# Optimization experiments

Hardware: AMD Instinct MI355X
Metric: run time of the kernel (lower is better)

The kernel has to match this reference:

```python
import jax, jax.numpy as jnp
import numpy as np

N = 50000        # nodes
E = 800000       # edges (before self-loops)
IN = 128         # in_channels
HID = 32         # hidden_channels
HEADS = 8        # num_heads
G = 64           # num graphs in batch
NEG_SLOPE = 0.2  # PyG GATConv default


def setup_inputs() -> dict:
    key = jax.random.key(0)
    ks = jax.random.split(key, 12)
    x = jax.random.normal(ks[0], (N, IN), jnp.float32)
    edge_index = jax.random.randint(ks[1], (2, E), 0, N, jnp.int32)
    edge_attr = jax.random.normal(ks[2], (E, 4), jnp.float32)
    batch = jnp.sort(jax.random.randint(ks[3], (N,), 0, G, jnp.int32))
    s = 0.05
    # GATConv 1: in -> HEADS*HID
    W1 = jax.random.normal(ks[4], (IN, HEADS * HID), jnp.float32) * s
    a_src1 = jax.random.normal(ks[5], (HEADS, HID), jnp.float32) * s
    a_dst1 = jax.random.normal(ks[6], (HEADS, HID), jnp.float32) * s
    b1 = jnp.zeros((HEADS * HID,), jnp.float32)
    # GATConv 2: HEADS*HID -> HID (heads=1)
    W2 = jax.random.normal(ks[7], (HEADS * HID, HID), jnp.float32) * s
    a_src2 = jax.random.normal(ks[8], (1, HID), jnp.float32) * s
    a_dst2 = jax.random.normal(ks[9], (1, HID), jnp.float32) * s
    b2 = jnp.zeros((HID,), jnp.float32)
    return {"x": x, "edge_index": edge_index, "edge_attr": edge_attr, "batch": batch,
            "W1": W1, "a_src1": a_src1, "a_dst1": a_dst1, "b1": b1,
            "W2": W2, "a_src2": a_src2, "a_dst2": a_dst2, "b2": b2}


def gat_conv(x, src, dst, W, a_src, a_dst, b):
    # x: [N, F_in]; W: [F_in, H*C]; a_src/a_dst: [H, C]
    H, C = a_src.shape
    h = (x @ W).reshape(N, H, C)                      # [N, H, C]
    al_s = jnp.einsum('nhc,hc->nh', h, a_src)         # [N, H]
    al_d = jnp.einsum('nhc,hc->nh', h, a_dst)
    e = jax.nn.leaky_relu(al_s[src] + al_d[dst], NEG_SLOPE)  # [Etot, H]
    # segment softmax over incoming edges of each dst node
    m = jax.ops.segment_max(e, dst, num_segments=N)
    p = jnp.exp(e - m[dst])
    z = jax.ops.segment_sum(p, dst, num_segments=N)
    alpha = p / z[dst]                                # [Etot, H]
    out = jax.ops.segment_sum(alpha[:, :, None] * h[src], dst, num_segments=N)
    return out.reshape(N, H * C) + b


def reference(x, edge_index, edge_attr, batch, W1, a_src1, a_dst1, b1, W2, a_src2, a_dst2, b2):
    # edge_attr is ignored: GATConv was built without edge_dim (PyG lin_edge=None).
    loops = jnp.arange(N, dtype=edge_index.dtype)     # PyG add_self_loops=True
    src = jnp.concatenate([edge_index[0], loops])
    dst = jnp.concatenate([edge_index[1], loops])
    h = jax.nn.relu(gat_conv(x, src, dst, W1, a_src1, a_dst1, b1))
    # dropout p=0.2 is identity in eval mode
    h = gat_conv(h, src, dst, W2, a_src2, a_dst2, b2)  # [N, HID]
    # global_mean_pool over graph ids
    sums = jax.ops.segment_sum(h, batch, num_segments=G)
    cnts = jax.ops.segment_sum(jnp.ones((N, 1), h.dtype), batch, num_segments=G)
    return sums / jnp.maximum(cnts, 1.0)              # [G, HID]
```

## Files before the change

### kernel.cpp

```cpp
#include <hip/hip_runtime.h>
#include <hip/hip_bf16.h>

#define NNODES 50000
#define NEDGES 800000
#define FIN 128
#define HID 32
#define HEADS 8
#define NG 64
#define NEG_SLOPE 0.2f
#define MAXDEG 64
#define NPX 6250

using bf16x8 = __attribute__((ext_vector_type(8))) short;
using f32x4  = __attribute__((ext_vector_type(4))) float;
using f32x2  = __attribute__((ext_vector_type(2))) float;

static __device__ __forceinline__ float leaky(float x) {
    return x > 0.f ? x : NEG_SLOPE * x;
}
static __device__ __forceinline__ unsigned short f2bf(float f) {
    unsigned int x = __float_as_uint(f);
    return (unsigned short)((x + 0x7FFFu + ((x >> 16) & 1u)) >> 16);
}
static __device__ __forceinline__ unsigned int pack2bf(float lo, float hi) {
    return (unsigned int)f2bf(lo) | ((unsigned int)f2bf(hi) << 16);
}
static __device__ __forceinline__ float bfl(unsigned int u) {
    return __uint_as_float(u << 16);
}
static __device__ __forceinline__ float bfh(unsigned int u) {
    return __uint_as_float(u & 0xFFFF0000u);
}
static __device__ __forceinline__ unsigned char f2fp8(float f) {
    return (unsigned char)(__builtin_amdgcn_cvt_pk_fp8_f32(f, f, 0, false) & 0xFF);
}

#define ZERO_BLOCKS 196
__global__ void zero_swz_kernel(int* __restrict__ cnt,
                                const float* __restrict__ W1, const float* __restrict__ W2,
                                const float* __restrict__ a_src1, const float* __restrict__ a_dst1,
                                unsigned short* __restrict__ w1s,
                                unsigned short* __restrict__ w2s,
                                unsigned short* __restrict__ w1al) {
    if (blockIdx.x < ZERO_BLOCKS) {
        int i = blockIdx.x * 256 + threadIdx.x;
        if (i < NNODES) cnt[i] = 0;
        return;
    }
    int idx = (blockIdx.x - ZERO_BLOCKS) * 256 + threadIdx.x;
    if (idx < 32768) {
        int j    = idx & 7;
        int lane = (idx >> 3) & 63;
        int ks   = (idx >> 9) & 3;
        int ct   = idx >> 11;
        int k = ks * 32 + (lane >> 4) * 8 + j;
        int n = ct * 16 + (lane & 15);
        w1s[idx] = f2bf(W1[k * 256 + n]);
    } else if (idx < 32768 + 8192) {
        int id2  = idx - 32768;
        int j    = id2 & 7;
        int lane = (id2 >> 3) & 63;
        int ks   = (id2 >> 9) & 7;
        int ct   = id2 >> 12;
        int k = ks * 32 + (lane >> 4) * 8 + j;
        int n = ct * 16 + (lane & 15);
        w2s[id2] = f2bf(W2[k * 32 + n]);
    } else if (idx < 32768 + 8192 + 2048) {
        int id3  = idx - 40960;
        int j    = id3 & 7;
        int lane = (id3 >> 3) & 63;
        int ks   = id3 >> 9;
        int k = ks * 32 + (lane >> 4) * 8 + j;
        int c = lane & 15;
        int h = c & 7;
        const float* av = (c < 8) ? a_src1 : a_dst1;
        float v = 0.f;
#pragma unroll 8
        for (int cc = 0; cc < 32; ++cc)
            v += W1[k * 256 + h * 32 + cc] * av[h * 32 + cc];
        w1al[id3] = f2bf(v);
    }
}

#define SCAT_GROUPS 782
__global__ void scatter_kernel(const int* __restrict__ ei, int* __restrict__ cnt,
                               unsigned short* __restrict__ csr) {
    int xcd = blockIdx.x & 7;
    int slice = blockIdx.x >> 3;
    int e4 = slice * 256 + threadIdx.x;
    int dlo = xcd * NPX;
    int dhi = dlo + NPX;
    if (e4 < NEDGES / 4) {
        int4 d = *(const int4*)(ei + NEDGES + e4 * 4);
        int4 s;
        bool a0 = d.x >= dlo && d.x < dhi;
        bool a1 = d.y >= dlo && d.y < dhi;
        bool a2 = d.z >= dlo && d.z < dhi;
        bool a3 = d.w >= dlo && d.w < dhi;
        if (a0 | a1 | a2 | a3) s = *(const int4*)(ei + e4 * 4);
        if (a0) { int p = atomicAdd(&cnt[d.x], 1); csr[(d.x << 6) + p] = (unsigned short)s.x; }
        if (a1) { int p = atomicAdd(&cnt[d.y], 1); csr[(d.y << 6) + p] = (unsigned short)s.y; }
        if (a2) { int p = atomicAdd(&cnt[d.z], 1); csr[(d.z << 6) + p] = (unsigned short)s.z; }
        if (a3) { int p = atomicAdd(&cnt[d.w], 1); csr[(d.w << 6) + p] = (unsigned short)s.w; }
    }
}

__global__ __launch_bounds__(256) void gemm1_mfma_kernel(const float* __restrict__ x,
                                                         const unsigned short* __restrict__ w1s,
                                                         const unsigned short* __restrict__ w1al,
                                                         unsigned char* __restrict__ h1f8,
                                                         float* __restrict__ al_s,
                                                         float* __restrict__ al_d) {
    int t = threadIdx.x;
    int w = t >> 6;
    int l = t & 63;
    int lane16 = l & 15, quad = l >> 4;

    bf16x8 bf[4][4];
    const bf16x8* wp = (const bf16x8*)w1s;
#pragma unroll
    for (int ct = 0; ct < 4; ++ct)
#pragma unroll
        for (int ks = 0; ks < 4; ++ks)
            bf[ct][ks] = wp[((w * 4 + ct) * 4 + ks) * 64 + l];

    bf16x8 bf_al[4];
    if (w == 0) {
        const bf16x8* ap = (const bf16x8*)w1al;
#pragma unroll
        for (int ks = 0; ks < 4; ++ks)
            bf_al[ks] = ap[ks * 64 + l];
    }

    int rbase = blockIdx.x * 64;
    for (int rg = 0; rg < 4; ++rg) {
        int row0 = rbase + rg * 16;
        int r = row0 + lane16;
        int r_eff = r < NNODES ? r : NNODES - 1;
        bf16x8 af[4];
#pragma unroll
        for (int ks = 0; ks < 4; ++ks) {
            const float* ap = x + (size_t)r_eff * FIN + ks * 32 + quad * 8;
            float4 a0 = *(const float4*)ap;
            float4 a1 = *(const float4*)(ap + 4);
            bf16x8 v;
            v[0] = (short)f2bf(a0.x); v[1] = (short)f2bf(a0.y);
            v[2] = (short)f2bf(a0.z); v[3] = (short)f2bf(a0.w);
            v[4] = (short)f2bf(a1.x); v[5] = (short)f2bf(a1.y);
            v[6] = (short)f2bf(a1.z); v[7] = (short)f2bf(a1.w);
            af[ks] = v;
        }
        f32x4 acc[4];
#pragma unroll
        for (int ct = 0; ct < 4; ++ct) acc[ct] = (f32x4){0.f, 0.f, 0.f, 0.f};
#pragma unroll
        for (int ks = 0; ks < 4; ++ks)
#pragma unroll
            for (int ct = 0; ct < 4; ++ct)
                acc[ct] = __builtin_amdgcn_mfma_f32_16x16x32_bf16(af[ks], bf[ct][ks], acc[ct], 0, 0, 0);

        if (w == 0) {
            f32x4 aal = (f32x4){0.f, 0.f, 0.f, 0.f};
#pragma unroll
            for (int ks = 0; ks < 4; ++ks)
                aal = __builtin_amdgcn_mfma_f32_16x16x32_bf16(af[ks], bf_al[ks], aal, 0, 0, 0);
#pragma unroll
            for (int reg = 0; reg < 4; ++reg) {
                int gr = row0 + quad * 4 + reg;
                if (gr < NNODES) {
                    if (lane16 < 8) al_s[gr * HEADS + lane16] = aal[reg];
                    else            al_d[gr * HEADS + lane16 - 8] = aal[reg];
                }
            }
        }

#pragma unroll
        for (int ct = 0; ct < 4; ++ct)
#pragma unroll
            for (int reg = 0; reg < 4; ++reg) {
                int gr = row0 + quad * 4 + reg;
                if (gr < NNODES)
                    h1f8[(size_t)gr * 256 + w * 64 + ct * 16 + lane16] = f2fp8(acc[ct][reg]);
            }
    }
}

#define G1_SLICES 782
__global__ __launch_bounds__(256) void gather1_kernel(const unsigned char* __restrict__ h1f8,
                                                      const float* __restrict__ al_s,
                                                      const float* __restrict__ al_d,
                                                      const int* __restrict__ cnt,
                                                      const unsigned short* __restrict__ csr,
                                                      const float* __restrict__ b1,
                                                      unsigned short* __restrict__ out1b) {
    int b = blockIdx.x;
    int xcd = b & 7;
    int slice = b >> 3;
    int t = threadIdx.x;
    int l = t & 63;
    int q = l & 31;
    int base = l & 32;
    int ln = slice * 8 + (t >> 5);
    if (ln >= NPX) return;
    int n = xcd * NPX + ln;
    int e_st = q >> 3;
    int h_st = q & 7;
    int h_f  = q >> 2;
    float ad_st = al_d[n * HEADS + h_st];

    float p = __expf(leaky(al_s[n * HEADS + h_f] + al_d[n * HEADS + h_f]));
    float z = p;
    f32x2 acc01, acc23, acc45, acc67;
    {
        uint2 v = *(const uint2*)(h1f8 + (size_t)n * 256 + q * 8);
        f32x2 pp = (f32x2){p, p};
        acc01 = pp * __builtin_amdgcn_cvt_pk_f32_fp8(v.x, false);
        acc23 = pp * __builtin_amdgcn_cvt_pk_f32_fp8(v.x, true);
        acc45 = pp * __builtin_amdgcn_cvt_pk_f32_fp8(v.y, false);
        acc67 = pp * __builtin_amdgcn_cvt_pk_f32_fp8(v.y, true);
    }

    int beg = n << 6;
    int dg  = cnt[n];
    int end = beg + dg;
    int   src_c = n;
    float pe_c  = 0.f;
    if (e_st < dg) {
        src_c = csr[beg + e_st];
        pe_c = __expf(leaky(al_s[src_c * HEADS + h_st] + ad_st));
    }
    for (int i = beg; i < end; i += 4) {
        int remn = end - (i + 4);
        int   src_n = n;
        float pe_n  = 0.f;
        if (e_st < remn) {
            src_n = csr[i + 4 + e_st];
            pe_n = __expf(leaky(al_s[src_n * HEADS + h_st] + ad_st));
        }
#pragma unroll
        for (int j = 0; j < 4; ++j) {
            int   sj  = __shfl(src_c, base + j * 8);
            float pej = __shfl(pe_c, base + j * 8 + h_f);
            uint2 v = *(const uint2*)(h1f8 + (size_t)sj * 256 + q * 8);
            z += pej;
            f32x2 pj = (f32x2){pej, pej};
            acc01 += pj * __builtin_amdgcn_cvt_pk_f32_fp8(v.x, false);
            acc23 += pj * __builtin_amdgcn_cvt_pk_f32_fp8(v.x, true);
            acc45 += pj * __builtin_amdgcn_cvt_pk_f32_fp8(v.y, false);
            acc67 += pj * __builtin_amdgcn_cvt_pk_f32_fp8(v.y, true);
        }
        src_c = src_n; pe_c = pe_n;
    }
    float inv = 1.0f / z;
    float4 b0 = *(const float4*)(b1 + q * 8);
    float4 b2 = *(const float4*)(b1 + q * 8 + 4);
    float o[8];
    o[0] = acc01[0] * inv + b0.x; o[1] = acc01[1] * inv + b0.y;
    o[2] = acc23[0] * inv + b0.z; o[3] = acc23[1] * inv + b0.w;
    o[4] = acc45[0] * inv + b2.x; o[5] = acc45[1] * inv + b2.y;
    o[6] = acc67[0] * inv + b2.z; o[7] = acc67[1] * inv + b2.w;
#pragma unroll
    for (int k = 0; k < 8; ++k) o[k] = o[k] > 0.f ? o[k] : 0.f;
    uint4 pk;
    pk.x = pack2bf(o[0], o[1]); pk.y = pack2bf(o[2], o[3]);
    pk.z = pack2bf(o[4], o[5]); pk.w = pack2bf(o[6], o[7]);
    *(uint4*)(out1b + (size_t)n * 256 + q * 8) = pk;
}

__global__ __launch_bounds__(256) void gemm2_mfma_kernel(const unsigned short* __restrict__ out1b,
                                                         const unsigned short* __restrict__ w2s,
                                                         const float* __restrict__ a_src,
                                                         const float* __restrict__ a_dst,
                                                         unsigned short* __restrict__ h2b,
                                                         float* __restrict__ al_s,
                                                         float* __restrict__ al_d) {
    int t = threadIdx.x;
    int w = t >> 6;
    int l = t & 63;
    int lane16 = l & 15, quad = l >> 4;

    bf16x8 bf[2][8];
    const bf16x8* wp = (const bf16x8*)w2s;
#pragma unroll
    for (int ct = 0; ct < 2; ++ct)
#pragma unroll
        for (int ks = 0; ks < 8; ++ks)
            bf[ct][ks] = wp[((ct * 8 + ks)) * 64 + l];

    float as_c[2], ad_c[2];
#pragma unroll
    for (int ct = 0; ct < 2; ++ct) {
        as_c[ct] = a_src[ct * 16 + lane16];
        ad_c[ct] = a_dst[ct * 16 + lane16];
    }

    int row0 = blockIdx.x * 64 + w * 16;
    int r = row0 + lane16;
    int r_eff = r < NNODES ? r : NNODES - 1;
    f32x4 acc[2];
    acc[0] = (f32x4){0.f, 0.f, 0.f, 0.f};
    acc[1] = (f32x4){0.f, 0.f, 0.f, 0.f};
#pragma unroll
    for (int ks = 0; ks < 8; ++ks) {
        bf16x8 af = *(const bf16x8*)(out1b + (size_t)r_eff * 256 + ks * 32 + quad * 8);
        acc[0] = __builtin_amdgcn_mfma_f32_16x16x32_bf16(af, bf[0][ks], acc[0], 0, 0, 0);
        acc[1] = __builtin_amdgcn_mfma_f32_16x16x32_bf16(af, bf[1][ks], acc[1], 0, 0, 0);
    }
#pragma unroll
    for (int reg = 0; reg < 4; ++reg) {
        int gr = row0 + quad * 4 + reg;
        if (gr < NNODES) {
            h2b[(size_t)gr * 32 + lane16]      = f2bf(acc[0][reg]);
            h2b[(size_t)gr * 32 + 16 + lane16] = f2bf(acc[1][reg]);
        }
        float ps = acc[0][reg] * as_c[0] + acc[1][reg] * as_c[1];
        float pd = acc[0][reg] * ad_c[0] + acc[1][reg] * ad_c[1];
#pragma unroll
        for (int m = 1; m < 16; m <<= 1) {
            ps += __shfl_xor(ps, m);
            pd += __shfl_xor(pd, m);
        }
        if (lane16 == 0 && gr < NNODES) {
            al_s[gr] = ps;
            al_d[gr] = pd;
        }
    }
}

#define G2_SLICES 391
__global__ __launch_bounds__(256) void gather2_kernel(const unsigned short* __restrict__ h2b,
                                                      const float* __restrict__ al_s,
                                                      const float* __restrict__ al_d,
                                                      const int* __restrict__ cnt,
                                                      const unsigned short* __restrict__ csr,
                                                      const float* __restrict__ b2,
                                                      float* __restrict__ out2) {
    int b = blockIdx.x;
    int xcd = b & 7;
    int slice = b >> 3;
    int t = threadIdx.x;
    int l = t & 63;
    int e_sl = l & 15;
    int base = l & 48;
    int c0 = (l & 15) * 2;
    int ln = slice * 16 + (t >> 4);
    if (ln >= NPX) return;
    int n = xcd * NPX + ln;

    float ad = al_d[n];
    float p = __expf(leaky(al_s[n] + ad));
    float z = p;
    float acc0, acc1;
    {
        unsigned int v = *(const unsigned int*)(h2b + (size_t)n * HID + c0);
        acc0 = p * bfl(v);
        acc1 = p * bfh(v);
    }
    int beg = n << 6;
    int dg  = cnt[n];
    int end = beg + dg;
    int   src_c = n;
    float pe_c  = 0.f;
    if (e_sl < dg) {
        src_c = csr[beg + e_sl];
        pe_c = __expf(leaky(al_s[src_c] + ad));
    }
    for (int i = beg; i < end; i += 16) {
        int remn = end - (i + 16);
        int   src_n = n;
        float pe_n  = 0.f;
        if (e_sl < remn) {
            src_n = csr[i + 16 + e_sl];
            pe_n = __expf(leaky(al_s[src_n] + ad));
        }
        int m = end - i < 16 ? end - i : 16;
        for (int j0 = 0; j0 < m; j0 += 8) {
#pragma unroll
            for (int jj = 0; jj < 8; ++jj) {
                int   sj  = __shfl(src_c, base + j0 + jj);
                float pej = __shfl(pe_c, base + j0 + jj);
                unsigned int v = *(const unsigned int*)(h2b + (size_t)sj * HID + c0);
                z += pej;
                acc0 += pej * bfl(v);
                acc1 += pej * bfh(v);
            }
        }
        src_c = src_n; pe_c = pe_n;
    }
    float inv = 1.0f / z;
    float2 o;
    o.x = acc0 * inv + b2[c0];
    o.y = acc1 * inv + b2[c0 + 1];
    *(float2*)(out2 + (size_t)n * HID + c0) = o;
}

__global__ __launch_bounds__(256) void pool_kernel(const float* __restrict__ out2,
                                                   const int* __restrict__ batch,
                                                   float* __restrict__ out) {
    __shared__ float red[256];
    int g = blockIdx.x;
    int t = threadIdx.x;
    int c = t & 31;
    int sub = t >> 5;
    int beg, end;
    {
        int lo = 0, hi = NNODES;
        while (lo < hi) { int mid = (lo + hi) >> 1; if (batch[mid] < g) lo = mid + 1; else hi = mid; }
        beg = lo;
        lo = beg; hi = NNODES;
        while (lo < hi) { int mid = (lo + hi) >> 1; if (batch[mid] < g + 1) lo = mid + 1; else hi = mid; }
        end = lo;
    }
    float s = 0.f;
    for (int n = beg + sub; n < end; n += 8) s += out2[n * HID + c];
    red[t] = s;
    __syncthreads();
    if (t < 32) {
        float tot = 0.f;
#pragma unroll
        for (int k = 0; k < 8; ++k) tot += red[c + 32 * k];
        int cnt2 = end - beg;
        out[g * HID + c] = tot / (float)(cnt2 > 0 ? cnt2 : 1);
    }
}

extern "C" void kernel_launch(void* const* d_in, const int* in_sizes, int n_in,
                              void* d_out, int out_size, void* d_ws, size_t ws_size,
                              hipStream_t stream) {
    const float* x      = (const float*)d_in[0];
    const int*   ei     = (const int*)d_in[1];
    const int*   batch  = (const int*)d_in[3];
    const float* W1     = (const float*)d_in[4];
    const float* a_src1 = (const float*)d_in[5];
    const float* a_dst1 = (const float*)d_in[6];
    const float* b1     = (const float*)d_in[7];
    const float* W2     = (const float*)d_in[8];
    const float* a_src2 = (const float*)d_in[9];
    const float* a_dst2 = (const float*)d_in[10];
    const float* b2     = (const float*)d_in[11];
    float* out = (float*)d_out;

    char* ws = (char*)d_ws;
    size_t off = 0;
    auto alloc = [&](size_t bytes) {
        size_t o = off;
        off = (off + bytes + 255) & ~(size_t)255;
        return o;
    };
    unsigned char*  h1f8  = (unsigned char*)(ws + alloc((size_t)NNODES * 256));
    unsigned short* out1b = (unsigned short*)(ws + alloc((size_t)NNODES * 256 * 2));
    unsigned short* h2b   = (unsigned short*)(ws + alloc((size_t)NNODES * HID * 2));
    unsigned short* w1s   = (unsigned short*)(ws + alloc((size_t)16 * 4 * 64 * 8 * 2));
    unsigned short* w2s   = (unsigned short*)(ws + alloc((size_t)2 * 8 * 64 * 8 * 2));
    unsigned short* w1al  = (unsigned short*)(ws + alloc((size_t)4 * 64 * 8 * 2));
    float* out2   = (float*)(ws + alloc((size_t)NNODES * HID * 4));
    float* al_s1  = (float*)(ws + alloc((size_t)NNODES * HEADS * 4));
    float* al_d1  = (float*)(ws + alloc((size_t)NNODES * HEADS * 4));
    float* al_s2  = (float*)(ws + alloc((size_t)NNODES * 4));
    float* al_d2  = (float*)(ws + alloc((size_t)NNODES * 4));
    int*   cnt    = (int*)(ws + alloc((size_t)NNODES * 4));
    unsigned short* csr = (unsigned short*)(ws + alloc((size_t)NNODES * MAXDEG * 2));
    (void)ws_size;

    zero_swz_kernel<<<ZERO_BLOCKS + 168, 256, 0, stream>>>(cnt, W1, W2, a_src1, a_dst1,
                                                           w1s, w2s, w1al);
    scatter_kernel<<<SCAT_GROUPS * 8, 256, 0, stream>>>(ei, cnt, csr);

    gemm1_mfma_kernel<<<(NNODES + 63) / 64, 256, 0, stream>>>(x, w1s, w1al,
                                                              h1f8, al_s1, al_d1);
    gather1_kernel<<<8 * G1_SLICES, 256, 0, stream>>>(h1f8, al_s1, al_d1, cnt, csr, b1, out1b);

    gemm2_mfma_kernel<<<(NNODES + 63) / 64, 256, 0, stream>>>(out1b, w2s, a_src2, a_dst2,
                                                              h2b, al_s2, al_d2);
    gather2_kernel<<<8 * G2_SLICES, 256, 0, stream>>>(h2b, al_s2, al_d2, cnt, csr, b2, out2);
    pool_kernel<<<NG, 256, 0, stream>>>(out2, batch, out);
}
```

Before: 252.9 us.

## Partition layer-1 features by head pairs so gather blocks touch one slice

The layer-1 projected features and attention logits are now stored head-pair-major: four slices of 64 bytes per node plus paired float2 logits. The gather kernel maps each block to one head pair and half of the node range, so each of the 8 block slots works over a 3.2 MB feature slice, which is meant to improve L2/cache locality per XCD. Each node is handled by 8 lanes processing 8 edges per step. The output is written with nontemporal stores. In exchange the CSR indices and counts are read four times, once per head pair, and each random gather is only 64 bytes.

```diff
diff --git a/kernel.cpp b/kernel.cpp
--- a/kernel.cpp
+++ b/kernel.cpp
@@ -10,10 +10,12 @@
 #define NEG_SLOPE 0.2f
 #define MAXDEG 64
 #define NPX 6250
+#define NHALF 25000
 
 using bf16x8 = __attribute__((ext_vector_type(8))) short;
 using f32x4  = __attribute__((ext_vector_type(4))) float;
 using f32x2  = __attribute__((ext_vector_type(2))) float;
+using u32x4  = __attribute__((ext_vector_type(4))) unsigned int;
 
 static __device__ __forceinline__ float leaky(float x) {
     return x > 0.f ? x : NEG_SLOPE * x;
@@ -108,9 +110,9 @@
 __global__ __launch_bounds__(256) void gemm1_mfma_kernel(const float* __restrict__ x,
                                                          const unsigned short* __restrict__ w1s,
                                                          const unsigned short* __restrict__ w1al,
-                                                         unsigned char* __restrict__ h1f8,
-                                                         float* __restrict__ al_s,
-                                                         float* __restrict__ al_d) {
+                                                         unsigned char* __restrict__ h1p,
+                                                         float* __restrict__ alp,
+                                                         float* __restrict__ adp) {
     int t = threadIdx.x;
     int w = t >> 6;
     int l = t & 63;
@@ -168,8 +170,13 @@
             for (int reg = 0; reg < 4; ++reg) {
                 int gr = row0 + quad * 4 + reg;
                 if (gr < NNODES) {
-                    if (lane16 < 8) al_s[gr * HEADS + lane16] = aal[reg];
-                    else            al_d[gr * HEADS + lane16 - 8] = aal[reg];
+                    if (lane16 < 8) {
+                        int h = lane16;
+                        alp[((size_t)(h >> 1) * NNODES + gr) * 2 + (h & 1)] = aal[reg];
+                    } else {
+                        int h = lane16 - 8;
+                        adp[((size_t)(h >> 1) * NNODES + gr) * 2 + (h & 1)] = aal[reg];
+                    }
                 }
             }
         }
@@ -180,39 +187,42 @@
             for (int reg = 0; reg < 4; ++reg) {
                 int gr = row0 + quad * 4 + reg;
                 if (gr < NNODES)
-                    h1f8[(size_t)gr * 256 + w * 64 + ct * 16 + lane16] = f2fp8(acc[ct][reg]);
+                    h1p[((size_t)w * NNODES + gr) * 64 + ct * 16 + lane16] = f2fp8(acc[ct][reg]);
             }
     }
 }
 
 #define G1_SLICES 782
-__global__ __launch_bounds__(256) void gather1_kernel(const unsigned char* __restrict__ h1f8,
-                                                      const float* __restrict__ al_s,
-                                                      const float* __restrict__ al_d,
+__global__ __launch_bounds__(256) void gather1_kernel(const unsigned char* __restrict__ h1p,
+                                                      const float* __restrict__ alp,
+                                                      const float* __restrict__ adp,
                                                       const int* __restrict__ cnt,
                                                       const unsigned short* __restrict__ csr,
                                                       const float* __restrict__ b1,
                                                       unsigned short* __restrict__ out1b) {
     int b = blockIdx.x;
-    int xcd = b & 7;
-    int slice = b >> 3;
+    int slot = b & 7;
+    int hp = slot >> 1;
+    int half = slot & 1;
     int t = threadIdx.x;
     int l = t & 63;
-    int q = l & 31;
-    int base = l & 32;
-    int ln = slice * 8 + (t >> 5);
-    if (ln >= NPX) return;
-    int n = xcd * NPX + ln;
-    int e_st = q >> 3;
-    int h_st = q & 7;
-    int h_f  = q >> 2;
-    float ad_st = al_d[n * HEADS + h_st];
-
-    float p = __expf(leaky(al_s[n * HEADS + h_f] + al_d[n * HEADS + h_f]));
+    int rr = l & 7;
+    int base = l & 56;
+    int hs = rr >> 2;
+    int n = half * NHALF + (b >> 3) * 32 + (t >> 3);
+    if (n >= NNODES) return;
+
+    const float* alh = alp + (size_t)hp * NNODES * 2;
+    float2 adv = *(const float2*)(adp + ((size_t)hp * NNODES + n) * 2);
+    float2 asv = *(const float2*)(alh + (size_t)n * 2);
+    const unsigned char* hrow = h1p + (size_t)hp * NNODES * 64;
+
+    float ad_me = hs ? adv.y : adv.x;
+    float p = __expf(leaky((hs ? asv.y : asv.x) + ad_me));
     float z = p;
     f32x2 acc01, acc23, acc45, acc67;
     {
-        uint2 v = *(const uint2*)(h1f8 + (size_t)n * 256 + q * 8);
+        uint2 v = *(const uint2*)(hrow + (size_t)n * 64 + rr * 8);
         f32x2 pp = (f32x2){p, p};
         acc01 = pp * __builtin_amdgcn_cvt_pk_f32_fp8(v.x, false);
         acc23 = pp * __builtin_amdgcn_cvt_pk_f32_fp8(v.x, true);
@@ -223,25 +233,31 @@
     int beg = n << 6;
     int dg  = cnt[n];
     int end = beg + dg;
-    int   src_c = n;
-    float pe_c  = 0.f;
-    if (e_st < dg) {
-        src_c = csr[beg + e_st];
-        pe_c = __expf(leaky(al_s[src_c * HEADS + h_st] + ad_st));
-    }
-    for (int i = beg; i < end; i += 4) {
-        int remn = end - (i + 4);
-        int   src_n = n;
-        float pe_n  = 0.f;
-        if (e_st < remn) {
-            src_n = csr[i + 4 + e_st];
-            pe_n = __expf(leaky(al_s[src_n * HEADS + h_st] + ad_st));
-        }
-#pragma unroll
-        for (int j = 0; j < 4; ++j) {
-            int   sj  = __shfl(src_c, base + j * 8);
-            float pej = __shfl(pe_c, base + j * 8 + h_f);
-            uint2 v = *(const uint2*)(h1f8 + (size_t)sj * 256 + q * 8);
+    int   sc = n;
+    float p0c = 0.f, p1c = 0.f;
+    if (rr < dg) {
+        sc = csr[beg + rr];
+        float2 av = *(const float2*)(alh + (size_t)sc * 2);
+        p0c = __expf(leaky(av.x + adv.x));
+        p1c = __expf(leaky(av.y + adv.y));
+    }
+    for (int i = beg; i < end; i += 8) {
+        int remn = end - (i + 8);
+        int   sn = n;
+        float p0n = 0.f, p1n = 0.f;
+        if (rr < remn) {
+            sn = csr[i + 8 + rr];
+            float2 av = *(const float2*)(alh + (size_t)sn * 2);
+            p0n = __expf(leaky(av.x + adv.x));
+            p1n = __expf(leaky(av.y + adv.y));
+        }
+#pragma unroll
+        for (int j = 0; j < 8; ++j) {
+            int   sj  = __shfl(sc, base + j);
+            float pj0 = __shfl(p0c, base + j);
+            float pj1 = __shfl(p1c, base + j);
+            float pej = hs ? pj1 : pj0;
+            uint2 v = *(const uint2*)(hrow + (size_t)sj * 64 + rr * 8);
             z += pej;
             f32x2 pj = (f32x2){pej, pej};
             acc01 += pj * __builtin_amdgcn_cvt_pk_f32_fp8(v.x, false);
@@ -249,11 +265,12 @@
             acc45 += pj * __builtin_amdgcn_cvt_pk_f32_fp8(v.y, false);
             acc67 += pj * __builtin_amdgcn_cvt_pk_f32_fp8(v.y, true);
         }
-        src_c = src_n; pe_c = pe_n;
+        sc = sn; p0c = p0n; p1c = p1n;
     }
     float inv = 1.0f / z;
-    float4 b0 = *(const float4*)(b1 + q * 8);
-    float4 b2 = *(const float4*)(b1 + q * 8 + 4);
+    int colb = hp * 64 + rr * 8;
+    float4 b0 = *(const float4*)(b1 + colb);
+    float4 b2 = *(const float4*)(b1 + colb + 4);
     float o[8];
     o[0] = acc01[0] * inv + b0.x; o[1] = acc01[1] * inv + b0.y;
     o[2] = acc23[0] * inv + b0.z; o[3] = acc23[1] * inv + b0.w;
@@ -261,10 +278,10 @@
     o[6] = acc67[0] * inv + b2.z; o[7] = acc67[1] * inv + b2.w;
 #pragma unroll
     for (int k = 0; k < 8; ++k) o[k] = o[k] > 0.f ? o[k] : 0.f;
-    uint4 pk;
-    pk.x = pack2bf(o[0], o[1]); pk.y = pack2bf(o[2], o[3]);
-    pk.z = pack2bf(o[4], o[5]); pk.w = pack2bf(o[6], o[7]);
-    *(uint4*)(out1b + (size_t)n * 256 + q * 8) = pk;
+    u32x4 pk;
+    pk[0] = pack2bf(o[0], o[1]); pk[1] = pack2bf(o[2], o[3]);
+    pk[2] = pack2bf(o[4], o[5]); pk[3] = pack2bf(o[6], o[7]);
+    __builtin_nontemporal_store(pk, (u32x4*)(out1b + (size_t)n * 256 + colb));
 }
 
 __global__ __launch_bounds__(256) void gemm2_mfma_kernel(const unsigned short* __restrict__ out1b,
@@ -447,15 +464,15 @@
         off = (off + bytes + 255) & ~(size_t)255;
         return o;
     };
-    unsigned char*  h1f8  = (unsigned char*)(ws + alloc((size_t)NNODES * 256));
+    unsigned char*  h1p   = (unsigned char*)(ws + alloc((size_t)NNODES * 256));
     unsigned short* out1b = (unsigned short*)(ws + alloc((size_t)NNODES * 256 * 2));
     unsigned short* h2b   = (unsigned short*)(ws + alloc((size_t)NNODES * HID * 2));
     unsigned short* w1s   = (unsigned short*)(ws + alloc((size_t)16 * 4 * 64 * 8 * 2));
     unsigned short* w2s   = (unsigned short*)(ws + alloc((size_t)2 * 8 * 64 * 8 * 2));
     unsigned short* w1al  = (unsigned short*)(ws + alloc((size_t)4 * 64 * 8 * 2));
     float* out2   = (float*)(ws + alloc((size_t)NNODES * HID * 4));
-    float* al_s1  = (float*)(ws + alloc((size_t)NNODES * HEADS * 4));
-    float* al_d1  = (float*)(ws + alloc((size_t)NNODES * HEADS * 4));
+    float* alp    = (float*)(ws + alloc((size_t)NNODES * HEADS * 4));
+    float* adp    = (float*)(ws + alloc((size_t)NNODES * HEADS * 4));
     float* al_s2  = (float*)(ws + alloc((size_t)NNODES * 4));
     float* al_d2  = (float*)(ws + alloc((size_t)NNODES * 4));
     int*   cnt    = (int*)(ws + alloc((size_t)NNODES * 4));
@@ -467,8 +484,8 @@
     scatter_kernel<<<SCAT_GROUPS * 8, 256, 0, stream>>>(ei, cnt, csr);
 
     gemm1_mfma_kernel<<<(NNODES + 63) / 64, 256, 0, stream>>>(x, w1s, w1al,
-                                                              h1f8, al_s1, al_d1);
-    gather1_kernel<<<8 * G1_SLICES, 256, 0, stream>>>(h1f8, al_s1, al_d1, cnt, csr, b1, out1b);
+                                                              h1p, alp, adp);
+    gather1_kernel<<<8 * G1_SLICES, 256, 0, stream>>>(h1p, alp, adp, cnt, csr, b1, out1b);
 
     gemm2_mfma_kernel<<<(NNODES + 63) / 64, 256, 0, stream>>>(out1b, w2s, a_src2, a_dst2,
                                                               h2b, al_s2, al_d2);
```

Measured after the change: 257.2 us. Within noise of the previous version (+1.7%).

## Replace shuffle-based edge distribution with per-lane vector CSR loads in gathers

Applied to the files above, without the earlier changes.

Both gather kernels drop the scheme where lanes cooperatively load CSR indices and attention logits and then broadcast them with shuffles, with prefetch of the next chunk. Each lane now loads 8 CSR entries as one 16-byte vector and computes its own attention weight per edge, guarding the tail with a predicate. This removes the shuffle traffic and prefetch bookkeeping. In exchange every lane redoes the al_s loads and exp computation per edge, and the software prefetch of the next chunk is gone.

```diff
diff --git a/kernel.cpp b/kernel.cpp
--- a/kernel.cpp
+++ b/kernel.cpp
@@ -14,6 +14,7 @@
 using bf16x8 = __attribute__((ext_vector_type(8))) short;
 using f32x4  = __attribute__((ext_vector_type(4))) float;
 using f32x2  = __attribute__((ext_vector_type(2))) float;
+using u16x8  = __attribute__((ext_vector_type(8))) unsigned short;
 
 static __device__ __forceinline__ float leaky(float x) {
     return x > 0.f ? x : NEG_SLOPE * x;
@@ -199,16 +200,13 @@
     int t = threadIdx.x;
     int l = t & 63;
     int q = l & 31;
-    int base = l & 32;
     int ln = slice * 8 + (t >> 5);
     if (ln >= NPX) return;
     int n = xcd * NPX + ln;
-    int e_st = q >> 3;
-    int h_st = q & 7;
-    int h_f  = q >> 2;
-    float ad_st = al_d[n * HEADS + h_st];
-
-    float p = __expf(leaky(al_s[n * HEADS + h_f] + al_d[n * HEADS + h_f]));
+    int h_f = q >> 2;
+    float ad_f = al_d[n * HEADS + h_f];
+
+    float p = __expf(leaky(al_s[n * HEADS + h_f] + ad_f));
     float z = p;
     f32x2 acc01, acc23, acc45, acc67;
     {
@@ -223,24 +221,14 @@
     int beg = n << 6;
     int dg  = cnt[n];
     int end = beg + dg;
-    int   src_c = n;
-    float pe_c  = 0.f;
-    if (e_st < dg) {
-        src_c = csr[beg + e_st];
-        pe_c = __expf(leaky(al_s[src_c * HEADS + h_st] + ad_st));
-    }
-    for (int i = beg; i < end; i += 4) {
-        int remn = end - (i + 4);
-        int   src_n = n;
-        float pe_n  = 0.f;
-        if (e_st < remn) {
-            src_n = csr[i + 4 + e_st];
-            pe_n = __expf(leaky(al_s[src_n * HEADS + h_st] + ad_st));
-        }
-#pragma unroll
-        for (int j = 0; j < 4; ++j) {
-            int   sj  = __shfl(src_c, base + j * 8);
-            float pej = __shfl(pe_c, base + j * 8 + h_f);
+    for (int i = beg; i < end; i += 8) {
+        u16x8 eb = *(const u16x8*)(csr + i);
+#pragma unroll
+        for (int j = 0; j < 8; ++j) {
+            bool act = (i + j) < end;
+            int sj = act ? (int)eb[j] : n;
+            float as = al_s[sj * HEADS + h_f];
+            float pej = act ? __expf(leaky(as + ad_f)) : 0.f;
             uint2 v = *(const uint2*)(h1f8 + (size_t)sj * 256 + q * 8);
             z += pej;
             f32x2 pj = (f32x2){pej, pej};
@@ -249,7 +237,6 @@
             acc45 += pj * __builtin_amdgcn_cvt_pk_f32_fp8(v.y, false);
             acc67 += pj * __builtin_amdgcn_cvt_pk_f32_fp8(v.y, true);
         }
-        src_c = src_n; pe_c = pe_n;
     }
     float inv = 1.0f / z;
     float4 b0 = *(const float4*)(b1 + q * 8);
@@ -340,8 +327,6 @@
     int slice = b >> 3;
     int t = threadIdx.x;
     int l = t & 63;
-    int e_sl = l & 15;
-    int base = l & 48;
     int c0 = (l & 15) * 2;
     int ln = slice * 16 + (t >> 4);
     if (ln >= NPX) return;
@@ -359,33 +344,19 @@
     int beg = n << 6;
     int dg  = cnt[n];
     int end = beg + dg;
-    int   src_c = n;
-    float pe_c  = 0.f;
-    if (e_sl < dg) {
-        src_c = csr[beg + e_sl];
-        pe_c = __expf(leaky(al_s[src_c] + ad));
-    }
-    for (int i = beg; i < end; i += 16) {
-        int remn = end - (i + 16);
-        int   src_n = n;
-        float pe_n  = 0.f;
-        if (e_sl < remn) {
-            src_n = csr[i + 16 + e_sl];
-            pe_n = __expf(leaky(al_s[src_n] + ad));
-        }
-        int m = end - i < 16 ? end - i : 16;
-        for (int j0 = 0; j0 < m; j0 += 8) {
-#pragma unroll
-            for (int jj = 0; jj < 8; ++jj) {
-                int   sj  = __shfl(src_c, base + j0 + jj);
-                float pej = __shfl(pe_c, base + j0 + jj);
-                unsigned int v = *(const unsigned int*)(h2b + (size_t)sj * HID + c0);
-                z += pej;
-                acc0 += pej * bfl(v);
-                acc1 += pej * bfh(v);
-            }
-        }
-        src_c = src_n; pe_c = pe_n;
+    for (int i = beg; i < end; i += 8) {
+        u16x8 eb = *(const u16x8*)(csr + i);
+#pragma unroll
+        for (int j = 0; j < 8; ++j) {
+            bool act = (i + j) < end;
+            int sj = act ? (int)eb[j] : n;
+            float as = al_s[sj];
+            float pej = act ? __expf(leaky(as + ad)) : 0.f;
+            unsigned int v = *(const unsigned int*)(h2b + (size_t)sj * HID + c0);
+            z += pej;
+            acc0 += pej * bfl(v);
+            acc1 += pej * bfh(v);
+        }
     }
     float inv = 1.0f / z;
     float2 o;
```

Result: slower. 269.5 us (+6.6%).
